# Kernel optimization log

Hardware: AMD Instinct MI355X
Metric: run time of the kernel (lower is better)

## Reference

```python
import jax, jax.numpy as jnp
import numpy as np
import math

B, L, DM = 2, 2048, 1536
H, FD = 12, 16          # num_heads, feature_dim
DV = DM // H            # head_dim = 128
D2 = FD * FD            # expanded Taylor feature dim = 256
CHUNK = 128
EPS = 1e-12
LN_EPS = 1e-5


def setup_inputs() -> dict:
    key = jax.random.key(0)
    ks = jax.random.split(key, 5)
    s = lambda fan_in: 1.0 / math.sqrt(fan_in)
    return {
        "hidden_states": jax.random.normal(ks[0], (B, L, DM), jnp.float32),
        "Wq": jax.random.normal(ks[1], (DM, H * FD), jnp.float32) * s(DM),
        "Wk": jax.random.normal(ks[2], (DM, H * FD), jnp.float32) * s(DM),
        "Wv": jax.random.normal(ks[3], (DM, H * DV), jnp.float32) * s(DM),
        "Wo": jax.random.normal(ks[4], (H * DV, DM), jnp.float32) * s(H * DV),
        "ln_q_g": jnp.ones((H * FD,), jnp.float32),
        "ln_q_b": jnp.zeros((H * FD,), jnp.float32),
        "ln_k_g": jnp.ones((H * FD,), jnp.float32),
        "ln_k_b": jnp.zeros((H * FD,), jnp.float32),
    }


def _layernorm(x, g, b):
    mu = x.mean(-1, keepdims=True)
    var = ((x - mu) ** 2).mean(-1, keepdims=True)
    return (x - mu) * jax.lax.rsqrt(var + LN_EPS) * g + b


def _taylor_exp(x):
    # x: (b, h, l, d) -> flattened outer product / sqrt(d): (b, h, l, d*d)
    x2 = x[..., :, None] * x[..., None, :]
    return x2.reshape(*x.shape[:-1], -1) / math.sqrt(FD)


def _rebased_forward(hidden_states, Wq, Wk, Wv, Wo, ln_q_g, ln_q_b, ln_k_g, ln_k_b):
    b, l, _ = hidden_states.shape
    q = _layernorm(hidden_states @ Wq, ln_q_g, ln_q_b)
    k = _layernorm(hidden_states @ Wk, ln_k_g, ln_k_b)
    v = hidden_states @ Wv
    # (b, l, h*d) -> (b, h, l, d)
    q = q.reshape(b, l, H, FD).transpose(0, 2, 1, 3)
    k = k.reshape(b, l, H, FD).transpose(0, 2, 1, 3)
    v = v.reshape(b, l, H, DV).transpose(0, 2, 1, 3)
    q2 = _taylor_exp(q)  # (b, h, l, D2)
    k2 = _taylor_exp(k)

    nC = l // CHUNK
    # chunk-major layout for scan: (nC, b, h, C, .)
    q2c = q2.reshape(b, H, nC, CHUNK, D2).transpose(2, 0, 1, 3, 4)
    k2c = k2.reshape(b, H, nC, CHUNK, D2).transpose(2, 0, 1, 3, 4)
    vc = v.reshape(b, H, nC, CHUNK, DV).transpose(2, 0, 1, 3, 4)
    mask = jnp.tril(jnp.ones((CHUNK, CHUNK), q2.dtype))  # causal within chunk

    S0 = jnp.zeros((b, H, D2, DV), q2.dtype)  # running sum of k2^T v
    z0 = jnp.zeros((b, H, D2), q2.dtype)      # running sum of k2

    def step(carry, inp):
        S, z = carry
        qc, kc, vcur = inp
        A = jnp.einsum("bhcd,bhed->bhce", qc, kc) * mask  # intra-chunk scores
        num = jnp.einsum("bhcd,bhdv->bhcv", qc, S) + jnp.einsum("bhce,bhev->bhcv", A, vcur)
        den = jnp.einsum("bhcd,bhd->bhc", qc, z) + A.sum(-1)
        o = num / (den[..., None] + EPS)
        S = S + jnp.einsum("bhed,bhev->bhdv", kc, vcur)
        z = z + kc.sum(2)
        return (S, z), o

    _, o = jax.lax.scan(step, (S0, z0), (q2c, k2c, vc))
    # (nC, b, h, C, dv) -> (b, l, h*dv)
    o = o.transpose(1, 2, 0, 3, 4).reshape(b, H, l, DV).transpose(0, 2, 1, 3).reshape(b, l, H * DV)
    return o @ Wo


def reference(hidden_states, Wq, Wk, Wv, Wo, ln_q_g, ln_q_b, ln_k_g, ln_k_b):
    return _rebased_forward(hidden_states, Wq, Wk, Wv, Wo, ln_q_g, ln_q_b, ln_k_g, ln_k_b)
```

## Files before the change

kernel.cpp:

```cpp
#include <hip/hip_runtime.h>
#include <hip/hip_bf16.h>
#include <math.h>

#define Bc   2
#define Lc   2048
#define DMc  1536
#define Hc   12
#define FDc  16
#define DVc  128
#define D2c  256
#define CHK  128
#define NCH  16
#define ROWS (Bc*Lc)
#define HFD  (Hc*FDc)
#define HDV  (Hc*DVc)
#define NQK  (2*HFD)
#define NPRJ (NQK + HDV)

typedef __bf16 bf16x8 __attribute__((ext_vector_type(8)));
typedef float f32x4 __attribute__((ext_vector_type(4)));

__device__ __forceinline__ float bf2f(unsigned short u) {
    return __uint_as_float(((unsigned int)u) << 16);
}
__device__ __forceinline__ unsigned short f2bf(float v) {
    unsigned int u = __float_as_uint(v);
    unsigned int r = (u + 0x7FFFu + ((u >> 16) & 1u)) >> 16;
    return (unsigned short)r;
}
__device__ __forceinline__ unsigned int pack2(unsigned short a, unsigned short b) {
    return (unsigned int)a | ((unsigned int)b << 16);
}
__device__ __forceinline__ float ldin(const void* p, size_t i, int isf32) {
    return isf32 ? ((const float*)p)[i] : bf2f(((const unsigned short*)p)[i]);
}

#define GLL16(g, l) __builtin_amdgcn_global_load_lds( \
    (const __attribute__((address_space(1))) unsigned int*)(g), \
    (__attribute__((address_space(3))) unsigned int*)(l), 16, 0, 0)

__global__ void probe_dtype(const unsigned short* __restrict__ hs, int* __restrict__ flag) {
    const int tid = threadIdx.x;
    int sane = 0;
    for (int i = tid; i < 1024; i += 256) {
        unsigned short b = hs[2 * i];
        int e = (b >> 7) & 0xFF;
        if (e >= 97 && e <= 157) sane++;
    }
    __shared__ int tot;
    if (tid == 0) tot = 0;
    __syncthreads();
    atomicAdd(&tot, sane);
    __syncthreads();
    if (tid == 0) *flag = (tot >= 614) ? 0 : 1;
}

__global__ __launch_bounds__(256) void conv_bf16(const void* __restrict__ X,
                                                 unsigned short* __restrict__ Y,
                                                 int n4, const int* __restrict__ flagp) {
    const int f = *flagp;
    int i = blockIdx.x * 256 + threadIdx.x;
    if (i >= n4) return;
    if (f) {
        float4 x = ((const float4*)X)[i];
        ushort4 y;
        y.x = f2bf(x.x); y.y = f2bf(x.y); y.z = f2bf(x.z); y.w = f2bf(x.w);
        ((ushort4*)Y)[i] = y;
    } else {
        ((ushort4*)Y)[i] = ((const ushort4*)X)[i];
    }
}

__global__ __launch_bounds__(256) void convT_bf16(const void* __restrict__ W,
                                                  unsigned short* __restrict__ Wt,
                                                  int rows, int cols,
                                                  const int* __restrict__ flagp) {
    const int f = *flagp;
    __shared__ float tile[64][65];
    const int t = threadIdx.x;
    const int bx = blockIdx.x * 64;
    const int by = blockIdx.y * 64;
#pragma unroll
    for (int u = 0; u < 16; u++) {
        int idx = t + u * 256;
        int r = idx >> 6, c = idx & 63;
        tile[r][c] = ldin(W, (size_t)(by + r) * cols + bx + c, f);
    }
    __syncthreads();
#pragma unroll
    for (int u = 0; u < 16; u++) {
        int idx = t + u * 256;
        int r = idx >> 6, c = idx & 63;
        Wt[(size_t)(bx + r) * rows + by + c] = f2bf(tile[c][r]);
    }
}

__global__ __launch_bounds__(256) void gemm_mfma_bt(const unsigned short* __restrict__ A,
                                                    const unsigned short* __restrict__ Bt,
                                                    void* __restrict__ C,
                                                    int M, int N, int K,
                                                    int ksplit, int ldc,
                                                    int cMode, const int* __restrict__ flagp,
                                                    unsigned short* __restrict__ vTout) {
    const int f = *flagp;
    __shared__ __align__(16) unsigned short As[128 * 32];
    __shared__ __align__(16) unsigned short Bs[128 * 32];
    const int tid = threadIdx.x;
    const int wave = tid >> 6, lane = tid & 63;
    const int row0 = blockIdx.y * 128, col0 = blockIdx.x * 128;
    const int wrow = (wave >> 1) * 64, wcol = (wave & 1) * 64;
    const int mlane = lane & 15, quad = lane >> 4;
    const int kStart = blockIdx.z * ksplit;

    const unsigned short* Ab = A + (size_t)row0 * K + kStart;
    const unsigned short* Bb = Bt + (size_t)col0 * K + kStart;
    const int r0 = tid >> 2;
    const int kc = (tid & 3) * 8;
    const size_t off0 = (size_t)r0 * K + kc;
    const size_t off1 = (size_t)(r0 + 64) * K + kc;
    char* AsW = (char*)As + wave * 1024;
    char* BsW = (char*)Bs + wave * 1024;

    f32x4 acc[4][4] = {};

    for (int k0 = 0; k0 < ksplit; k0 += 32) {
        GLL16(Ab + off0 + k0, AsW);
        GLL16(Ab + off1 + k0, AsW + 4096);
        GLL16(Bb + off0 + k0, BsW);
        GLL16(Bb + off1 + k0, BsW + 4096);
        __syncthreads();
        bf16x8 a[4], b[4];
#pragma unroll
        for (int i = 0; i < 4; i++)
            a[i] = *(const bf16x8*)&As[(wrow + i * 16 + mlane) * 32 + quad * 8];
#pragma unroll
        for (int j = 0; j < 4; j++)
            b[j] = *(const bf16x8*)&Bs[(wcol + j * 16 + mlane) * 32 + quad * 8];
#pragma unroll
        for (int i = 0; i < 4; i++)
#pragma unroll
            for (int j = 0; j < 4; j++)
                acc[i][j] = __builtin_amdgcn_mfma_f32_16x16x32_bf16(a[i], b[j], acc[i][j], 0, 0, 0);
        __syncthreads();
    }

    float* Cf = nullptr;
    unsigned short* Cb16 = nullptr;
    bool doT = false;
    int tOff = 0;
    if (cMode == 0) Cf = (float*)C;
    else if (cMode == 1) Cb16 = (unsigned short*)C;
    else if (cMode == 2) { if (f) Cf = (float*)C; else Cb16 = (unsigned short*)C; }
    else if (cMode == 4) {
        if (col0 < NQK) Cf = (float*)C;
        else { doT = true; tOff = NQK; }
    }
    else if (cMode == 5) Cf = (float*)C + (size_t)blockIdx.z * ((size_t)M * N);
    if (cMode <= 3 && vTout) doT = true;

#pragma unroll
    for (int i = 0; i < 4; i++)
#pragma unroll
        for (int j = 0; j < 4; j++) {
            const int col = col0 + wcol + j * 16 + mlane;
            if (Cf) {
#pragma unroll
                for (int r = 0; r < 4; r++) {
                    const int row = row0 + wrow + i * 16 + quad * 4 + r;
                    Cf[(size_t)row * ldc + col] = acc[i][j][r];
                }
            } else if (Cb16) {
#pragma unroll
                for (int r = 0; r < 4; r++) {
                    const int row = row0 + wrow + i * 16 + quad * 4 + r;
                    Cb16[(size_t)row * ldc + col] = f2bf(acc[i][j][r]);
                }
            }
            if (doT) {
                ushort4 pk;
                pk.x = f2bf(acc[i][j][0]); pk.y = f2bf(acc[i][j][1]);
                pk.z = f2bf(acc[i][j][2]); pk.w = f2bf(acc[i][j][3]);
                *(ushort4*)(vTout + (size_t)(col - tOff) * M + row0 + wrow + i * 16 + quad * 4) = pk;
            }
        }
}

__global__ __launch_bounds__(256) void reduce_out(const float* __restrict__ P,
                                                  void* __restrict__ out,
                                                  int n4, const int* __restrict__ flagp) {
    const int f = *flagp;
    int i = blockIdx.x * 256 + threadIdx.x;
    if (i >= n4) return;
    const size_t n = (size_t)ROWS * DMc;
    float4 a = ((const float4*)P)[i];
    float4 b = ((const float4*)(P + n))[i];
    a.x += b.x; a.y += b.y; a.z += b.z; a.w += b.w;
    if (f) {
        ((float4*)out)[i] = a;
    } else {
        ushort4 y;
        y.x = f2bf(a.x); y.y = f2bf(a.y); y.z = f2bf(a.z); y.w = f2bf(a.w);
        ((ushort4*)out)[i] = y;
    }
}

__global__ __launch_bounds__(192) void ln_kernel(const float* __restrict__ qk,
                                                 float* __restrict__ q, float* __restrict__ k,
                                                 const void* __restrict__ gq,
                                                 const void* __restrict__ bq,
                                                 const void* __restrict__ gk,
                                                 const void* __restrict__ bk,
                                                 const int* __restrict__ flagp) {
    const int f = *flagp;
    const int row = blockIdx.x, t = threadIdx.x;
    float vq = qk[(size_t)row * NQK + t];
    float vk = qk[(size_t)row * NQK + HFD + t];
    float s[4] = {vq, vq * vq, vk, vk * vk};
    __shared__ float part[4][3];
    const int w = t >> 6, lane = t & 63;
#pragma unroll
    for (int i = 0; i < 4; i++) {
        float v = s[i];
        for (int off = 32; off; off >>= 1) v += __shfl_down(v, off);
        if (lane == 0) part[i][w] = v;
    }
    __syncthreads();
    float sq  = part[0][0] + part[0][1] + part[0][2];
    float sq2 = part[1][0] + part[1][1] + part[1][2];
    float sk  = part[2][0] + part[2][1] + part[2][2];
    float sk2 = part[3][0] + part[3][1] + part[3][2];
    const float inv = 1.0f / (float)HFD;
    float muq = sq * inv, muk = sk * inv;
    float varq = sq2 * inv - muq * muq;
    float vark = sk2 * inv - muk * muk;
    float oq = (vq - muq) * rsqrtf(varq + 1e-5f) * ldin(gq, t, f) + ldin(bq, t, f);
    float ok = (vk - muk) * rsqrtf(vark + 1e-5f) * ldin(gk, t, f) + ldin(bk, t, f);
    q[(size_t)row * HFD + t] = oq;
    k[(size_t)row * HFD + t] = ok;
}

__global__ __launch_bounds__(256) void state_prefix_mfma(const float* __restrict__ kn,
                                                         const unsigned short* __restrict__ vT,
                                                         unsigned short* __restrict__ St,
                                                         float* __restrict__ zc) {
    const int bx = blockIdx.x;
    const int by = blockIdx.y;
    const int bh = blockIdx.z;
    const int h = bh % Hc, b = bh / Hc;
    const int t0 = bx * 16;
    const int tid = threadIdx.x;
    const int wave = tid >> 6, lane = tid & 63;
    const int mlane = lane & 15, quad = lane >> 4;

    __shared__ __align__(16) float kcs[CHK * FDc];
    __shared__ __align__(16) unsigned short K2t[16 * 136];
    __shared__ __align__(16) unsigned short Vs[64 * 136];
    __shared__ float zp[16][17];
    __shared__ float zpre[16];
    if (tid < 16) zpre[tid] = 0.f;

    f32x4 acc = {};
    const int kr = tid >> 1, khf = tid & 1;
    const int d2l = tid & 15, cg = tid >> 4;
    const int vrow = tid >> 2, vseg = tid & 3;
    const int dvL = wave * 16 + mlane;

    for (int n = 0; n < NCH; n++) {
        const int row0 = b * Lc + n * CHK;
        __syncthreads();
        {
            const float4* src = (const float4*)(kn + (size_t)(row0 + kr) * HFD + h * FDc + khf * 8);
            *(float4*)(kcs + kr * 16 + khf * 8)     = src[0];
            *(float4*)(kcs + kr * 16 + khf * 8 + 4) = src[1];
            const uint4* g = (const uint4*)(vT + (size_t)(h * 128 + by * 64 + vrow) * ROWS + row0 + vseg * 32);
            *(uint4*)(Vs + vrow * 136 + vseg * 32)      = g[0];
            *(uint4*)(Vs + vrow * 136 + vseg * 32 + 8)  = g[1];
            *(uint4*)(Vs + vrow * 136 + vseg * 32 + 16) = g[2];
            *(uint4*)(Vs + vrow * 136 + vseg * 32 + 24) = g[3];
        }
        __syncthreads();
        {
            float zs_ = 0.f;
            unsigned short pk[8];
#pragma unroll
            for (int u = 0; u < 8; u++) {
                int c = cg * 8 + u;
                float p = kcs[c * 16 + bx] * kcs[c * 16 + d2l] * 0.25f;
                zs_ += p;
                pk[u] = f2bf(p);
            }
            uint4 w;
            w.x = pack2(pk[0], pk[1]); w.y = pack2(pk[2], pk[3]);
            w.z = pack2(pk[4], pk[5]); w.w = pack2(pk[6], pk[7]);
            *(uint4*)(K2t + d2l * 136 + cg * 8) = w;
            zp[d2l][cg] = zs_;
        }
        __syncthreads();
        {
            size_t base = (((size_t)(bh * NCH + n) * 16 + bx) * 128) * 16;
            int dv = by * 64 + dvL;
            ushort4 pk;
            pk.x = f2bf(acc[0]); pk.y = f2bf(acc[1]);
            pk.z = f2bf(acc[2]); pk.w = f2bf(acc[3]);
            *(ushort4*)(St + base + (size_t)dv * 16 + quad * 4) = pk;
            if (tid < 16) {
                float s = 0.f;
#pragma unroll
                for (int c = 0; c < 16; c++) s += zp[tid][c];
                if (by == 0)
                    zc[(size_t)(bh * NCH + n) * D2c + t0 + tid] = zpre[tid];
                zpre[tid] += s;
            }
        }
        {
#pragma unroll
            for (int ks = 0; ks < 4; ks++) {
                bf16x8 a = *(const bf16x8*)(K2t + mlane * 136 + ks * 32 + quad * 8);
                bf16x8 bfr = *(const bf16x8*)(Vs + dvL * 136 + ks * 32 + quad * 8);
                acc = __builtin_amdgcn_mfma_f32_16x16x32_bf16(a, bfr, acc, 0, 0, 0);
            }
        }
    }
}

__global__ __launch_bounds__(256) void chunk_out_mfma(const float* __restrict__ qn,
                                                      const float* __restrict__ kn,
                                                      const unsigned short* __restrict__ St,
                                                      const float* __restrict__ z,
                                                      const unsigned short* __restrict__ vT,
                                                      unsigned short* __restrict__ o) {
    const int blk = blockIdx.x;
    const int n = blk & 15, bh = blk >> 4;
    const int h = bh % Hc, b = bh / Hc;
    const int row0 = b * Lc + n * CHK;
    const int tid = threadIdx.x;
    const int wave = tid >> 6, lane = tid & 63;
    const int mlane = lane & 15, quad = lane >> 4;
    const int wrow = (wave >> 1) * 64, wcol = (wave & 1) * 64;

    __shared__ __align__(16) unsigned char lds[61952];
    float* Qs   = (float*)lds;
    float* zs   = (float*)(lds + 8192);
    float* denp = (float*)(lds + 9216);
    float* dinv = (float*)(lds + 10240);
    unsigned char* U = lds + 10752;
    unsigned short* Q2s = (unsigned short*)U;
    unsigned short* Sts = (unsigned short*)(U + 10240);
    unsigned short* Kb  = (unsigned short*)U;
    unsigned short* Qb  = (unsigned short*)(U + 8192);
    unsigned short* At  = (unsigned short*)(U + 16384);
    unsigned short* Vs  = (unsigned short*)U;

    {
        int r = tid >> 1, hf = tid & 1;
        const float4* src = (const float4*)(qn + (size_t)(row0 + r) * HFD + h * FDc + hf * 8);
        *(float4*)(Qs + r * 16 + hf * 8)     = src[0];
        *(float4*)(Qs + r * 16 + hf * 8 + 4) = src[1];
        if (tid < 64)
            ((float4*)zs)[tid] = ((const float4*)(z + ((size_t)bh * NCH + n) * D2c))[tid];
    }
    __syncthreads();

    const int qc = tid >> 1, qhalf = tid & 1;
    float qr[16];
#pragma unroll
    for (int ff = 0; ff < 16; ff++) qr[ff] = Qs[qc * 16 + ff];

    f32x4 acc[4][4] = {};
    float den1 = 0.f;
    const unsigned short* Stb = St + ((size_t)bh * NCH + n) * ((size_t)D2c * DVc);

    for (int k0 = 0; k0 < 256; k0 += 32) {
        {
            unsigned short pk[16];
#pragma unroll
            for (int kk = 0; kk < 16; kk++) {
                int d2 = k0 + qhalf * 16 + kk;
                float val = qr[d2 >> 4] * qr[d2 & 15] * 0.25f;
                den1 += val * zs[d2];
                pk[kk] = f2bf(val);
            }
            uint4 w0, w1;
            w0.x = pack2(pk[0], pk[1]);  w0.y = pack2(pk[2], pk[3]);
            w0.z = pack2(pk[4], pk[5]);  w0.w = pack2(pk[6], pk[7]);
            w1.x = pack2(pk[8], pk[9]);  w1.y = pack2(pk[10], pk[11]);
            w1.z = pack2(pk[12], pk[13]); w1.w = pack2(pk[14], pk[15]);
            *(uint4*)(Q2s + qc * 40 + qhalf * 16) = w0;
            *(uint4*)(Q2s + qc * 40 + qhalf * 16 + 8) = w1;
        }
        {
            int r = tid >> 1, hf = tid & 1;
            const uint4* g = (const uint4*)(Stb + (size_t)((k0 >> 4) + hf) * 2048 + r * 16);
            uint4 d0 = g[0], d1 = g[1];
            *(uint4*)(Sts + r * 40 + hf * 16) = d0;
            *(uint4*)(Sts + r * 40 + hf * 16 + 8) = d1;
        }
        __syncthreads();
        bf16x8 a[4], bfr[4];
#pragma unroll
        for (int i = 0; i < 4; i++)
            a[i] = *(const bf16x8*)(Q2s + (wrow + i * 16 + mlane) * 40 + quad * 8);
#pragma unroll
        for (int j = 0; j < 4; j++)
            bfr[j] = *(const bf16x8*)(Sts + (wcol + j * 16 + mlane) * 40 + quad * 8);
#pragma unroll
        for (int i = 0; i < 4; i++)
#pragma unroll
            for (int j = 0; j < 4; j++)
                acc[i][j] = __builtin_amdgcn_mfma_f32_16x16x32_bf16(a[i], bfr[j], acc[i][j], 0, 0, 0);
        __syncthreads();
    }
    denp[qhalf * 128 + qc] = den1;

    {
        int r = tid >> 1, hf = tid & 1;
        if (hf == 0) {
            unsigned short pq[16], pkk[16];
#pragma unroll
            for (int ff = 0; ff < 16; ff++) pq[ff] = f2bf(Qs[r * 16 + ff]);
            const float* kg = kn + (size_t)(row0 + r) * HFD + h * FDc;
#pragma unroll
            for (int ff = 0; ff < 16; ff++) pkk[ff] = f2bf(kg[ff]);
            uint4 w;
            w.x = pack2(pq[0], pq[1]);  w.y = pack2(pq[2], pq[3]);
            w.z = pack2(pq[4], pq[5]);  w.w = pack2(pq[6], pq[7]);
            *(uint4*)(Qb + r * 32) = w;
            w.x = pack2(pq[8], pq[9]);  w.y = pack2(pq[10], pq[11]);
            w.z = pack2(pq[12], pq[13]); w.w = pack2(pq[14], pq[15]);
            *(uint4*)(Qb + r * 32 + 8) = w;
            w.x = pack2(pkk[0], pkk[1]);  w.y = pack2(pkk[2], pkk[3]);
            w.z = pack2(pkk[4], pkk[5]);  w.w = pack2(pkk[6], pkk[7]);
            *(uint4*)(Kb + r * 32) = w;
            w.x = pack2(pkk[8], pkk[9]);  w.y = pack2(pkk[10], pkk[11]);
            w.z = pack2(pkk[12], pkk[13]); w.w = pack2(pkk[14], pkk[15]);
            *(uint4*)(Kb + r * 32 + 8) = w;
        } else {
            uint4 zz = make_uint4(0, 0, 0, 0);
            *(uint4*)(Qb + r * 32 + 16) = zz;
            *(uint4*)(Qb + r * 32 + 24) = zz;
            *(uint4*)(Kb + r * 32 + 16) = zz;
            *(uint4*)(Kb + r * 32 + 24) = zz;
        }
    }
    __syncthreads();

    {
        f32x4 pacc[4][4] = {};
        bf16x8 a[4], bfr[4];
#pragma unroll
        for (int i = 0; i < 4; i++)
            a[i] = *(const bf16x8*)(Qb + (wrow + i * 16 + mlane) * 32 + quad * 8);
#pragma unroll
        for (int j = 0; j < 4; j++)
            bfr[j] = *(const bf16x8*)(Kb + (wcol + j * 16 + mlane) * 32 + quad * 8);
#pragma unroll
        for (int i = 0; i < 4; i++)
#pragma unroll
            for (int j = 0; j < 4; j++)
                pacc[i][j] = __builtin_amdgcn_mfma_f32_16x16x32_bf16(a[i], bfr[j], pacc[i][j], 0, 0, 0);
#pragma unroll
        for (int i = 0; i < 4; i++)
#pragma unroll
            for (int j = 0; j < 4; j++) {
                int e = wcol + j * 16 + mlane;
#pragma unroll
                for (int r = 0; r < 4; r++) {
                    int c = wrow + i * 16 + quad * 4 + r;
                    float p = pacc[i][j][r];
                    float aval = (e <= c) ? p * p * 0.0625f : 0.f;
                    At[c * 136 + e] = f2bf(aval);
                }
            }
    }
    __syncthreads();

    if (tid < 128) {
        float rs = 0.f;
#pragma unroll
        for (int e8 = 0; e8 < 128; e8 += 8) {
            bf16x8 v8 = *(const bf16x8*)(At + tid * 136 + e8);
#pragma unroll
            for (int u = 0; u < 8; u++) rs += (float)v8[u];
        }
        dinv[tid] = 1.0f / (denp[tid] + denp[128 + tid] + rs + 1e-12f);
    }

    for (int e0 = 0; e0 < 128; e0 += 32) {
        {
            int r = tid >> 1, hf = tid & 1;
            const uint4* g = (const uint4*)(vT + (size_t)(h * 128 + r) * ROWS + row0 + e0 + hf * 16);
            uint4 d0 = g[0], d1 = g[1];
            *(uint4*)(Vs + r * 40 + hf * 16) = d0;
            *(uint4*)(Vs + r * 40 + hf * 16 + 8) = d1;
        }
        __syncthreads();
        bf16x8 a[4], bfr[4];
#pragma unroll
        for (int i = 0; i < 4; i++)
            a[i] = *(const bf16x8*)(At + (wrow + i * 16 + mlane) * 136 + e0 + quad * 8);
#pragma unroll
        for (int j = 0; j < 4; j++)
            bfr[j] = *(const bf16x8*)(Vs + (wcol + j * 16 + mlane) * 40 + quad * 8);
#pragma unroll
        for (int i = 0; i < 4; i++)
#pragma unroll
            for (int j = 0; j < 4; j++)
                acc[i][j] = __builtin_amdgcn_mfma_f32_16x16x32_bf16(a[i], bfr[j], acc[i][j], 0, 0, 0);
        __syncthreads();
    }

#pragma unroll
    for (int i = 0; i < 4; i++)
#pragma unroll
        for (int j = 0; j < 4; j++) {
            int col = h * 128 + wcol + j * 16 + mlane;
#pragma unroll
            for (int r = 0; r < 4; r++) {
                int c = wrow + i * 16 + quad * 4 + r;
                o[(size_t)(row0 + c) * HDV + col] = f2bf(acc[i][j][r] * dinv[c]);
            }
        }
}

extern "C" void kernel_launch(void* const* d_in, const int* in_sizes, int n_in,
                              void* d_out, int out_size, void* d_ws, size_t ws_size,
                              hipStream_t stream) {
    const void* hs = d_in[0];
    const void* Wq = d_in[1];
    const void* Wk = d_in[2];
    const void* Wv = d_in[3];
    const void* Wo = d_in[4];
    const void* gq = d_in[5];
    const void* bq = d_in[6];
    const void* gk = d_in[7];
    const void* bk = d_in[8];

    int* flag = (int*)d_ws;
    float* base = (float*)d_ws + 16;
    float* qpre = base;
    float* kpre = qpre + (size_t)ROWS * HFD;
    float* vreg = kpre + (size_t)ROWS * HFD;
    float* Sc   = vreg + (size_t)ROWS * HDV;
    float* zc   = Sc + (size_t)Bc * Hc * NCH * D2c * DVc;
    float* fend = zc + (size_t)Bc * Hc * NCH * D2c;
    unsigned short* hsb = (unsigned short*)fend;
    unsigned short* ob  = hsb;
    unsigned short* Wot = hsb + (size_t)ROWS * DMc;
    unsigned short* vT  = Wot + (size_t)HDV * DMc;
    float* qk = Sc;
    unsigned short* Wqkvt = (unsigned short*)(Sc + (size_t)ROWS * NQK);
    float* Pout = Sc;
    unsigned short* St = (unsigned short*)vreg;

    probe_dtype<<<1, 256, 0, stream>>>((const unsigned short*)hs, flag);

    conv_bf16<<<(ROWS * DMc / 4 + 255) / 256, 256, 0, stream>>>(hs, hsb, ROWS * DMc / 4, flag);
    convT_bf16<<<dim3(HFD / 64, DMc / 64), 256, 0, stream>>>(Wq, Wqkvt, DMc, HFD, flag);
    convT_bf16<<<dim3(HFD / 64, DMc / 64), 256, 0, stream>>>(Wk, Wqkvt + (size_t)HFD * DMc, DMc, HFD, flag);
    convT_bf16<<<dim3(HDV / 64, DMc / 64), 256, 0, stream>>>(Wv, Wqkvt + (size_t)NQK * DMc, DMc, HDV, flag);
    convT_bf16<<<dim3(DMc / 64, HDV / 64), 256, 0, stream>>>(Wo, Wot, HDV, DMc, flag);

    gemm_mfma_bt<<<dim3(NPRJ / 128, ROWS / 128, 1), 256, 0, stream>>>(
        hsb, Wqkvt, qk, ROWS, NPRJ, DMc, DMc, NQK, 4, flag, vT);

    ln_kernel<<<ROWS, HFD, 0, stream>>>(qk, qpre, kpre, gq, bq, gk, bk, flag);

    state_prefix_mfma<<<dim3(16, 2, Bc * Hc), 256, 0, stream>>>(kpre, vT, St, zc);

    chunk_out_mfma<<<Bc * Hc * NCH, 256, 0, stream>>>(qpre, kpre, St, zc, vT, ob);

    gemm_mfma_bt<<<dim3(DMc / 128, ROWS / 128, 2), 256, 0, stream>>>(
        ob, Wot, Pout, ROWS, DMc, HDV, HDV / 2, DMc, 5, flag, nullptr);
    reduce_out<<<(ROWS * DMc / 4 + 255) / 256, 256, 0, stream>>>(Pout, d_out, ROWS * DMc / 4, flag);
}
```

Baseline: 292.6 us.

## Split K inside each GEMM block across two wave groups, drop reduce kernel

The bf16 MFMA GEMM now runs 512 threads per block. Two groups of four waves each handle half of the K dimension, and their partial accumulators are summed through LDS before the epilogue. This replaces the global split-K of the output projection, which wrote fp32 partial tiles to memory and then ran a separate reduce_out pass. That removes a large round trip of fp32 partials and one kernel launch, and gives the QKV projection more waves per tile. The cost is a 32KB LDS footprint, extra barriers for the staged reduction, and possibly lower block occupancy.

```diff
diff --git a/kernel.cpp b/kernel.cpp
--- a/kernel.cpp
+++ b/kernel.cpp
@@ -95,35 +95,42 @@
     }
 }
 
-__global__ __launch_bounds__(256) void gemm_mfma_bt(const unsigned short* __restrict__ A,
+__global__ __launch_bounds__(512) void gemm_mfma_bt(const unsigned short* __restrict__ A,
                                                     const unsigned short* __restrict__ Bt,
                                                     void* __restrict__ C,
                                                     int M, int N, int K,
-                                                    int ksplit, int ldc,
+                                                    int ldc,
                                                     int cMode, const int* __restrict__ flagp,
                                                     unsigned short* __restrict__ vTout) {
     const int f = *flagp;
-    __shared__ __align__(16) unsigned short As[128 * 32];
-    __shared__ __align__(16) unsigned short Bs[128 * 32];
+    __shared__ __align__(16) unsigned char smem[32768];
+    unsigned short* As = (unsigned short*)smem;
+    unsigned short* Bsu = As + 8192;
+    f32x4* scr4 = (f32x4*)smem;
+
     const int tid = threadIdx.x;
     const int wave = tid >> 6, lane = tid & 63;
+    const int kgrp = wave >> 2;
+    const int w4 = wave & 3;
     const int row0 = blockIdx.y * 128, col0 = blockIdx.x * 128;
-    const int wrow = (wave >> 1) * 64, wcol = (wave & 1) * 64;
+    const int wrow = (w4 >> 1) * 64, wcol = (w4 & 1) * 64;
     const int mlane = lane & 15, quad = lane >> 4;
-    const int kStart = blockIdx.z * ksplit;
-
-    const unsigned short* Ab = A + (size_t)row0 * K + kStart;
-    const unsigned short* Bb = Bt + (size_t)col0 * K + kStart;
-    const int r0 = tid >> 2;
-    const int kc = (tid & 3) * 8;
+    const int kHalf = K >> 1;
+
+    const unsigned short* Ab = A + (size_t)row0 * K + (size_t)kgrp * kHalf;
+    const unsigned short* Bb = Bt + (size_t)col0 * K + (size_t)kgrp * kHalf;
+    const int t256 = tid & 255;
+    const int r0 = t256 >> 2;
+    const int kc = (t256 & 3) * 8;
     const size_t off0 = (size_t)r0 * K + kc;
     const size_t off1 = (size_t)(r0 + 64) * K + kc;
-    char* AsW = (char*)As + wave * 1024;
-    char* BsW = (char*)Bs + wave * 1024;
+    char* AsW = (char*)As + kgrp * 8192 + w4 * 1024;
+    char* BsW = (char*)Bsu + kgrp * 8192 + w4 * 1024;
+    const int ldsBase = kgrp * 4096;
 
     f32x4 acc[4][4] = {};
 
-    for (int k0 = 0; k0 < ksplit; k0 += 32) {
+    for (int k0 = 0; k0 < kHalf; k0 += 32) {
         GLL16(Ab + off0 + k0, AsW);
         GLL16(Ab + off1 + k0, AsW + 4096);
         GLL16(Bb + off0 + k0, BsW);
@@ -132,10 +139,10 @@
         bf16x8 a[4], b[4];
 #pragma unroll
         for (int i = 0; i < 4; i++)
-            a[i] = *(const bf16x8*)&As[(wrow + i * 16 + mlane) * 32 + quad * 8];
+            a[i] = *(const bf16x8*)&As[ldsBase + (wrow + i * 16 + mlane) * 32 + quad * 8];
 #pragma unroll
         for (int j = 0; j < 4; j++)
-            b[j] = *(const bf16x8*)&Bs[(wcol + j * 16 + mlane) * 32 + quad * 8];
+            b[j] = *(const bf16x8*)&Bsu[ldsBase + (wcol + j * 16 + mlane) * 32 + quad * 8];
 #pragma unroll
         for (int i = 0; i < 4; i++)
 #pragma unroll
@@ -143,6 +150,42 @@
                 acc[i][j] = __builtin_amdgcn_mfma_f32_16x16x32_bf16(a[i], b[j], acc[i][j], 0, 0, 0);
         __syncthreads();
     }
+
+    {
+        const int col = (wave & 1) * 64 + lane;
+        if (kgrp == 1 && w4 < 2) {
+#pragma unroll
+            for (int i = 0; i < 4; i++)
+#pragma unroll
+                for (int j = 0; j < 4; j++)
+                    scr4[(i * 4 + j) * 128 + col] = acc[i][j];
+        }
+        __syncthreads();
+        if (kgrp == 0 && w4 < 2) {
+#pragma unroll
+            for (int i = 0; i < 4; i++)
+#pragma unroll
+                for (int j = 0; j < 4; j++)
+                    acc[i][j] += scr4[(i * 4 + j) * 128 + col];
+        }
+        __syncthreads();
+        if (kgrp == 1 && w4 >= 2) {
+#pragma unroll
+            for (int i = 0; i < 4; i++)
+#pragma unroll
+                for (int j = 0; j < 4; j++)
+                    scr4[(i * 4 + j) * 128 + col] = acc[i][j];
+        }
+        __syncthreads();
+        if (kgrp == 0 && w4 >= 2) {
+#pragma unroll
+            for (int i = 0; i < 4; i++)
+#pragma unroll
+                for (int j = 0; j < 4; j++)
+                    acc[i][j] += scr4[(i * 4 + j) * 128 + col];
+        }
+    }
+    if (kgrp != 0) return;
 
     float* Cf = nullptr;
     unsigned short* Cb16 = nullptr;
@@ -155,7 +198,6 @@
         if (col0 < NQK) Cf = (float*)C;
         else { doT = true; tOff = NQK; }
     }
-    else if (cMode == 5) Cf = (float*)C + (size_t)blockIdx.z * ((size_t)M * N);
     if (cMode <= 3 && vTout) doT = true;
 
 #pragma unroll
@@ -183,25 +225,6 @@
                 *(ushort4*)(vTout + (size_t)(col - tOff) * M + row0 + wrow + i * 16 + quad * 4) = pk;
             }
         }
-}
-
-__global__ __launch_bounds__(256) void reduce_out(const float* __restrict__ P,
-                                                  void* __restrict__ out,
-                                                  int n4, const int* __restrict__ flagp) {
-    const int f = *flagp;
-    int i = blockIdx.x * 256 + threadIdx.x;
-    if (i >= n4) return;
-    const size_t n = (size_t)ROWS * DMc;
-    float4 a = ((const float4*)P)[i];
-    float4 b = ((const float4*)(P + n))[i];
-    a.x += b.x; a.y += b.y; a.z += b.z; a.w += b.w;
-    if (f) {
-        ((float4*)out)[i] = a;
-    } else {
-        ushort4 y;
-        y.x = f2bf(a.x); y.y = f2bf(a.y); y.z = f2bf(a.z); y.w = f2bf(a.w);
-        ((ushort4*)out)[i] = y;
-    }
 }
 
 __global__ __launch_bounds__(192) void ln_kernel(const float* __restrict__ qk,
@@ -549,7 +572,6 @@
     unsigned short* vT  = Wot + (size_t)HDV * DMc;
     float* qk = Sc;
     unsigned short* Wqkvt = (unsigned short*)(Sc + (size_t)ROWS * NQK);
-    float* Pout = Sc;
     unsigned short* St = (unsigned short*)vreg;
 
     probe_dtype<<<1, 256, 0, stream>>>((const unsigned short*)hs, flag);
@@ -560,8 +582,8 @@
     convT_bf16<<<dim3(HDV / 64, DMc / 64), 256, 0, stream>>>(Wv, Wqkvt + (size_t)NQK * DMc, DMc, HDV, flag);
     convT_bf16<<<dim3(DMc / 64, HDV / 64), 256, 0, stream>>>(Wo, Wot, HDV, DMc, flag);
 
-    gemm_mfma_bt<<<dim3(NPRJ / 128, ROWS / 128, 1), 256, 0, stream>>>(
-        hsb, Wqkvt, qk, ROWS, NPRJ, DMc, DMc, NQK, 4, flag, vT);
+    gemm_mfma_bt<<<dim3(NPRJ / 128, ROWS / 128), 512, 0, stream>>>(
+        hsb, Wqkvt, qk, ROWS, NPRJ, DMc, NQK, 4, flag, vT);
 
     ln_kernel<<<ROWS, HFD, 0, stream>>>(qk, qpre, kpre, gq, bq, gk, bk, flag);
 
@@ -569,7 +591,6 @@
 
     chunk_out_mfma<<<Bc * Hc * NCH, 256, 0, stream>>>(qpre, kpre, St, zc, vT, ob);
 
-    gemm_mfma_bt<<<dim3(DMc / 128, ROWS / 128, 2), 256, 0, stream>>>(
-        ob, Wot, Pout, ROWS, DMc, HDV, HDV / 2, DMc, 5, flag, nullptr);
-    reduce_out<<<(ROWS * DMc / 4 + 255) / 256, 256, 0, stream>>>(Pout, d_out, ROWS * DMc / 4, flag);
-}
+    gemm_mfma_bt<<<dim3(DMc / 128, ROWS / 128), 512, 0, stream>>>(
+        ob, Wot, d_out, ROWS, DMc, HDV, DMc, 2, flag, nullptr);
+}
```

Result: faster. 270.4 us (-7.6%).
